# Optimization experiments

Hardware: AMD Instinct MI355X
Metric: run time of the kernel (lower is better)

Reference implementation:

```python
import jax, jax.numpy as jnp
import numpy as np

B, S, D, H = 4, 2048, 1024, 16
DEPTH = D // H
NEG = -1e10
BN_EPS = 1e-3


def setup_inputs() -> dict:
    key = jax.random.key(0)
    ks = jax.random.split(key, 6)
    scale = 0.02
    return {
        "x": jax.random.normal(ks[0], (B, S, D), dtype=jnp.float32),
        "mask": jax.random.randint(ks[1], (B, 1, 1, S), 0, 2, dtype=jnp.int32),
        "W_q": jax.random.normal(ks[2], (D, D), dtype=jnp.float32) * scale,
        "W_k": jax.random.normal(ks[3], (D, D), dtype=jnp.float32) * scale,
        "W_v": jax.random.normal(ks[4], (D, D), dtype=jnp.float32) * scale,
        "W_o": jax.random.normal(ks[5], (D, D), dtype=jnp.float32) * scale,
        "b_o": jnp.zeros((D,), dtype=jnp.float32),
        "gamma": jnp.ones((D,), dtype=jnp.float32),
        "beta": jnp.zeros((D,), dtype=jnp.float32),
        "moving_mean": jnp.zeros((D,), dtype=jnp.float32),
        "moving_var": jnp.ones((D,), dtype=jnp.float32),
    }


def _split_heads(t):
    # [B, S, D] -> [B, H, S, depth]
    return t.reshape(B, S, H, DEPTH).transpose(0, 2, 1, 3)


def reference(x, mask, W_q, W_k, W_v, W_o, b_o, gamma, beta, moving_mean, moving_var):
    Q = _split_heads(jnp.einsum("bsd,de->bse", x, W_q))
    K = _split_heads(jnp.einsum("bsd,de->bse", x, W_k))
    V = _split_heads(jnp.einsum("bsd,de->bse", x, W_v))
    # NOTE: scale is sqrt(EMBEDDING_SIZE), matching the original (not sqrt(depth)).
    scores = jnp.einsum("bhqd,bhkd->bhqk", Q, K) / jnp.sqrt(jnp.float32(D))
    # multiplicative mask: positions where mask==0 are multiplied by -1e10
    invalid = jnp.where(mask == 0, jnp.float32(NEG), jnp.float32(1.0))
    scores = scores * invalid
    attn = jax.nn.softmax(scores, axis=-1)
    out = jnp.einsum("bhqk,bhkd->bhqd", attn, V)
    out = out.transpose(0, 2, 1, 3).reshape(B, S, D)  # merge heads
    out = jnp.einsum("bsd,de->bse", out, W_o) + b_o
    # Keras BatchNormalization, inference mode (default call w/o training flag)
    out = gamma * (out - moving_mean) * jax.lax.rsqrt(moving_var + BN_EPS) + beta
    return out
```

## Files before the change

### kernel.cpp

```cpp
#include <hip/hip_runtime.h>
#include <hip/hip_bf16.h>
#include <float.h>

#define BB 4
#define SS 2048
#define DD 1024
#define HH 16
#define DP 64
#define BKS 32
#define MARGIN_F 0.025f
#define TIER2_TAU 1e-4

typedef __attribute__((ext_vector_type(8))) _Float16 half8v;
typedef __attribute__((ext_vector_type(16))) float f32x16;

typedef __attribute__((address_space(3))) void lds_void;
typedef const __attribute__((address_space(1))) void gbl_void;
static __device__ __forceinline__ void gload16(const void* g, void* l) {
  __builtin_amdgcn_global_load_lds((gbl_void*)g, (lds_void*)l, 16, 0, 0);
}

__global__ __launch_bounds__(256) void wtrans_kernel(
    const float* __restrict__ Wq, const float* __restrict__ Wk,
    const float* __restrict__ Wv, const float* __restrict__ Wo,
    _Float16* __restrict__ Wqh, _Float16* __restrict__ Wql,
    _Float16* __restrict__ Wkh, _Float16* __restrict__ Wkl,
    _Float16* __restrict__ Wvh, _Float16* __restrict__ Woh)
{
  const int z = blockIdx.z;
  const float* __restrict__ src = (z == 0) ? Wq : (z == 1 ? Wk : (z == 2 ? Wv : Wo));
  _Float16* __restrict__ dh = (z == 0) ? Wqh : (z == 1 ? Wkh : (z == 2 ? Wvh : Woh));
  _Float16* __restrict__ dl = (z == 0) ? Wql : Wkl;
  __shared__ float tile[64][65];
  const int k0 = blockIdx.x * 64, n0 = blockIdx.y * 64;
  const int c = threadIdx.x & 63, rb = threadIdx.x >> 6;
  #pragma unroll
  for (int i = 0; i < 16; ++i)
    tile[rb + 4 * i][c] = src[(size_t)(k0 + rb + 4 * i) * DD + n0 + c];
  __syncthreads();
  #pragma unroll
  for (int i = 0; i < 16; ++i) {
    const int n = n0 + rb + 4 * i;
    const float v = tile[c][rb + 4 * i];
    const _Float16 h = (_Float16)v;
    dh[(size_t)n * DD + k0 + c] = h;
    if (z < 2) dl[(size_t)n * DD + k0 + c] = (_Float16)(v - (float)h);
  }
}

__global__ __launch_bounds__(256) void proj_mfma(
    const float* __restrict__ x,
    const _Float16* __restrict__ Wqh, const _Float16* __restrict__ Wql,
    const _Float16* __restrict__ Wkh, const _Float16* __restrict__ Wkl,
    const _Float16* __restrict__ Wvh,
    _Float16* __restrict__ Qhi, _Float16* __restrict__ Qlo,
    _Float16* __restrict__ Khi, _Float16* __restrict__ Klo,
    _Float16* __restrict__ Vh)
{
  const int z = blockIdx.z;
  const bool split = (z < 2);
  const _Float16* __restrict__ Wh = (z == 0) ? Wqh : (z == 1 ? Wkh : Wvh);
  const _Float16* __restrict__ Wl = (z == 0) ? Wql : Wkl;
  _Float16* __restrict__ dhi = (z == 0) ? Qhi : (z == 1 ? Khi : Vh);
  _Float16* __restrict__ dlo = (z == 0) ? Qlo : Klo;

  __shared__ _Float16 Asm[8192];
  __shared__ _Float16 Bsm[8192];

  const int rows0 = blockIdx.x * 128, cols0 = blockIdx.y * 128;
  const int t = threadIdx.x;
  const int wid = t >> 6, l = t & 63;
  const int warpR = wid >> 1, warpC = wid & 1;
  const int lr = l & 31, lh = l >> 5;

  f32x16 acc[2][2];
  #pragma unroll
  for (int i = 0; i < 2; ++i)
    #pragma unroll
    for (int j = 0; j < 2; ++j)
      #pragma unroll
      for (int r = 0; r < 16; ++r) acc[i][j][r] = 0.f;

  const int arow = t >> 1;
  const int kc0 = (t & 1) * 2;
  const float* xsrc = x + (size_t)(rows0 + arow) * DD + kc0 * 8;
  int aslot_h0, aslot_h1, aslot_l0, aslot_l1;
  if (split) {
    aslot_h0 = arow * 8 + ((2 * kc0) ^ (arow & 7));
    aslot_h1 = arow * 8 + ((2 * kc0 + 2) ^ (arow & 7));
    aslot_l0 = arow * 8 + ((2 * kc0 + 1) ^ (arow & 7));
    aslot_l1 = arow * 8 + ((2 * kc0 + 3) ^ (arow & 7));
  } else {
    aslot_h0 = arow * 4 + (kc0 ^ ((arow >> 1) & 3));
    aslot_h1 = arow * 4 + ((kc0 + 1) ^ ((arow >> 1) & 3));
    aslot_l0 = aslot_l1 = 0;
  }

  const int nbi = split ? 4 : 2;
  const _Float16* bsrc[4];
  #pragma unroll
  for (int i = 0; i < 4; ++i) {
    const int s = t + i * 256;
    int col, wsrc; const _Float16* base;
    if (split) {
      col = s >> 3;
      const int u = (s & 7) ^ (col & 7);
      wsrc = u >> 1;
      base = (u & 1) ? Wl : Wh;
    } else {
      col = (s & 511) >> 2;
      wsrc = (s & 3) ^ ((col >> 1) & 3);
      base = Wh;
    }
    bsrc[i] = base + (size_t)(cols0 + col) * DD + wsrc * 8;
  }

  for (int ks = 0; ks < 32; ++ks) {
    const int k0 = ks * BKS;
    if (ks) __syncthreads();

    #pragma unroll
    for (int i = 0; i < 4; ++i)
      if (i < nbi) gload16(bsrc[i] + k0, &Bsm[(t + i * 256) * 8]);

    {
      const float4 f0 = *(const float4*)(xsrc + k0);
      const float4 f1 = *(const float4*)(xsrc + k0 + 4);
      const float4 f2 = *(const float4*)(xsrc + k0 + 8);
      const float4 f3 = *(const float4*)(xsrc + k0 + 12);
      const float xv[16] = {f0.x, f0.y, f0.z, f0.w, f1.x, f1.y, f1.z, f1.w,
                            f2.x, f2.y, f2.z, f2.w, f3.x, f3.y, f3.z, f3.w};
      half8v h0, h1, lo0, lo1;
      #pragma unroll
      for (int j = 0; j < 8; ++j) {
        h0[j] = (_Float16)xv[j];
        lo0[j] = (_Float16)(xv[j] - (float)h0[j]);
        h1[j] = (_Float16)xv[8 + j];
        lo1[j] = (_Float16)(xv[8 + j] - (float)h1[j]);
      }
      *(half8v*)&Asm[aslot_h0 * 8] = h0;
      *(half8v*)&Asm[aslot_h1 * 8] = h1;
      if (split) {
        *(half8v*)&Asm[aslot_l0 * 8] = lo0;
        *(half8v*)&Asm[aslot_l1 * 8] = lo1;
      }
    }
    __syncthreads();

    #pragma unroll
    for (int kh2 = 0; kh2 < 2; ++kh2) {
      const int c = kh2 * 2 + lh;
      half8v ah[2], alv[2], bh[2], blv[2];
      #pragma unroll
      for (int wr = 0; wr < 2; ++wr) {
        const int row = warpR * 64 + wr * 32 + lr;
        if (split) {
          ah[wr]  = *(const half8v*)&Asm[(row * 8 + ((2 * c) ^ (row & 7))) * 8];
          alv[wr] = *(const half8v*)&Asm[(row * 8 + ((2 * c + 1) ^ (row & 7))) * 8];
        } else {
          ah[wr] = *(const half8v*)&Asm[(row * 4 + (c ^ ((row >> 1) & 3))) * 8];
        }
      }
      #pragma unroll
      for (int wc = 0; wc < 2; ++wc) {
        const int col = warpC * 64 + wc * 32 + lr;
        if (split) {
          bh[wc]  = *(const half8v*)&Bsm[(col * 8 + ((2 * c) ^ (col & 7))) * 8];
          blv[wc] = *(const half8v*)&Bsm[(col * 8 + ((2 * c + 1) ^ (col & 7))) * 8];
        } else {
          bh[wc] = *(const half8v*)&Bsm[(col * 4 + (c ^ ((col >> 1) & 3))) * 8];
        }
      }
      #pragma unroll
      for (int wr = 0; wr < 2; ++wr)
        #pragma unroll
        for (int wc = 0; wc < 2; ++wc) {
          acc[wr][wc] = __builtin_amdgcn_mfma_f32_32x32x16_f16(ah[wr], bh[wc], acc[wr][wc], 0, 0, 0);
          if (split) {
            acc[wr][wc] = __builtin_amdgcn_mfma_f32_32x32x16_f16(alv[wr], bh[wc], acc[wr][wc], 0, 0, 0);
            acc[wr][wc] = __builtin_amdgcn_mfma_f32_32x32x16_f16(ah[wr], blv[wc], acc[wr][wc], 0, 0, 0);
          }
        }
    }
  }

  const int mb0 = rows0 + warpR * 64 + 4 * lh;
  #pragma unroll
  for (int wr = 0; wr < 2; ++wr)
    #pragma unroll
    for (int wc = 0; wc < 2; ++wc) {
      const int n = cols0 + warpC * 64 + wc * 32 + lr;
      const int h = n >> 6, d = n & 63;
      #pragma unroll
      for (int r = 0; r < 16; ++r) {
        const int m = mb0 + wr * 32 + (r & 3) + 8 * (r >> 2);
        const int b = m >> 11, srow = m & 2047;
        const size_t o = ((size_t)(b * HH + h) * SS + srow) * DP + d;
        const float a = acc[wr][wc][r];
        const _Float16 h16 = (_Float16)a;
        dhi[o] = h16;
        if (split) dlo[o] = (_Float16)(a - (float)h16);
      }
    }
}

__global__ __launch_bounds__(256) void scan_kernel(
    const int* __restrict__ mask, int* __restrict__ klist,
    int* __restrict__ cntpad, int* __restrict__ cntreal)
{
  __shared__ int part[256];
  __shared__ int tot;
  const int b = blockIdx.x, t = threadIdx.x;
  int loc[8]; int c = 0;
  #pragma unroll
  for (int j = 0; j < 8; ++j) {
    loc[j] = (mask[(b << 11) + t * 8 + j] == 0);
    c += loc[j];
  }
  part[t] = c;
  __syncthreads();
  if (t == 0) {
    int run = 0;
    for (int i = 0; i < 256; ++i) { int v = part[i]; part[i] = run; run += v; }
    tot = run;
  }
  __syncthreads();
  int off = part[t];
  #pragma unroll
  for (int j = 0; j < 8; ++j)
    if (loc[j]) klist[(b << 11) + off++] = t * 8 + j;
  __syncthreads();
  if (t == 0) {
    int n = tot;
    int first;
    if (n == 0) { klist[b << 11] = 0; n = 1; first = 0; }
    else first = klist[b << 11];
    int np = (n + 31) & ~31;
    for (int i = n; i < np; ++i) klist[(b << 11) + i] = first;
    cntpad[b] = np;
    cntreal[b] = n;
  }
}

__global__ __launch_bounds__(256) void filter_kernel(
    const _Float16* __restrict__ Qhi, const _Float16* __restrict__ Qlo,
    const _Float16* __restrict__ Khi,
    const int* __restrict__ klist, const int* __restrict__ cntpad,
    const int* __restrict__ cntreal,
    int* __restrict__ idx, int* __restrict__ ambr, int* __restrict__ ambc,
    int* __restrict__ cand, int* __restrict__ ccnt)
{
  __shared__ _Float16 Ksm[2048];
  const int bh = blockIdx.x >> 4;
  const int b = bh >> 4;
  const int wid = threadIdx.x >> 6;
  const int t = threadIdx.x;
  const int l = t & 63;
  const int q0 = ((blockIdx.x & 15) << 7) + (wid << 5);
  const int half = l >> 5;
  const int lq = l & 31;
  const int* __restrict__ kl_b = klist + (b << 11);

  half8v qh[4], ql[4];
  {
    const size_t qrow = ((size_t)bh * SS + q0 + lq) * DP + half * 8;
    #pragma unroll
    for (int ds = 0; ds < 4; ++ds) {
      qh[ds] = *(const half8v*)(Qhi + qrow + ds * 16);
      ql[ds] = *(const half8v*)(Qlo + qrow + ds * 16);
    }
  }

  const int srow = t >> 3;
  const int sslot = t & 7;
  const int scc = sslot ^ (srow & 7);

  const int nreal = cntreal[b];
  const int nt = cntpad[b] >> 5;
  float m1 = FLT_MAX, m2 = FLT_MAX, m3 = FLT_MAX, m4 = FLT_MAX;
  uint kidx[16];
  #pragma unroll
  for (int r = 0; r < 16; ++r)
    kidx[r] = (uint)((r & 3) + ((r >> 2) << 3) + (half << 2));

  const size_t kbase = (size_t)bh * SS;
  for (int kt = 0; kt < nt; ++kt) {
    if (kt) __syncthreads();
    {
      const int kval = kl_b[(kt << 5) + srow];
      gload16(Khi + (kbase + kval) * DP + scc * 8, &Ksm[t * 8]);
    }
    __syncthreads();

    f32x16 acc;
    #pragma unroll
    for (int r = 0; r < 16; ++r) acc[r] = 0.f;
    #pragma unroll
    for (int ds = 0; ds < 4; ++ds) {
      const int cc = ds * 2 + half;
      const int sl = lq * 8 + (cc ^ (lq & 7));
      const half8v kh = *(const half8v*)&Ksm[sl * 8];
      acc = __builtin_amdgcn_mfma_f32_32x32x16_f16(kh, qh[ds], acc, 0, 0, 0);
      acc = __builtin_amdgcn_mfma_f32_32x32x16_f16(kh, ql[ds], acc, 0, 0, 0);
    }
    const bool part = (kt == nt - 1) && ((nreal & 31) != 0);
    #pragma unroll
    for (int r = 0; r < 16; ++r) {
      const uint pv = (__float_as_uint(acc[r]) & 0xFFFFF800u) | kidx[r];
      float v = __uint_as_float(pv);
      if (part && kidx[r] >= (uint)nreal) v = FLT_MAX;
      m4 = __builtin_amdgcn_fmed3f(v, m3, m4);
      m3 = __builtin_amdgcn_fmed3f(v, m2, m3);
      m2 = __builtin_amdgcn_fmed3f(v, m1, m2);
      m1 = fminf(v, m1);
      kidx[r] += 32;
    }
  }

  float om[4];
  om[0] = __shfl_xor(m1, 32, 64);
  om[1] = __shfl_xor(m2, 32, 64);
  om[2] = __shfl_xor(m3, 32, 64);
  om[3] = __shfl_xor(m4, 32, 64);
  #pragma unroll
  for (int j = 0; j < 4; ++j) {
    const float v = om[j];
    m4 = __builtin_amdgcn_fmed3f(v, m3, m4);
    m3 = __builtin_amdgcn_fmed3f(v, m2, m3);
    m2 = __builtin_amdgcn_fmed3f(v, m1, m2);
    m1 = fminf(v, m1);
  }

  if (half == 0) {
    const int row = bh * SS + q0 + lq;
    const uint u1 = __float_as_uint(m1);
    const int k1 = kl_b[u1 & 2047u];
    idx[row] = k1;
    const float v1 = __uint_as_float(u1 & 0xFFFFF800u);
    const uint us[3] = {__float_as_uint(m2), __float_as_uint(m3),
                        __float_as_uint(m4)};
    const float v2 = __uint_as_float(us[0] & 0xFFFFF800u);
    if (v2 - v1 < MARGIN_F) {
      int c[4]; int n = 0;
      c[n++] = k1;
      #pragma unroll
      for (int j = 0; j < 3; ++j) {
        const float vj = __uint_as_float(us[j] & 0xFFFFF800u);
        if (vj - v1 < MARGIN_F) c[n++] = kl_b[us[j] & 2047u];
        else break;
      }
      const int pos = atomicAdd(ambc, 1);
      ambr[pos] = row;
      ccnt[row] = n;
      for (int j = 0; j < n; ++j) cand[row * 8 + j] = c[j];
    }
  }
}

__global__ __launch_bounds__(256) void refine_kernel(
    const _Float16* __restrict__ Qhi, const _Float16* __restrict__ Qlo,
    const _Float16* __restrict__ Khi, const _Float16* __restrict__ Klo,
    const float* __restrict__ x, const float* __restrict__ Wq,
    const float* __restrict__ Wk,
    const int* __restrict__ ambr, const int* __restrict__ ambc,
    const int* __restrict__ cand, const int* __restrict__ ccnt,
    int* __restrict__ idx)
{
  __shared__ double red[4][7][64];
  const int n = *ambc;
  const int t = threadIdx.x;
  const int w = t >> 6, lane = t & 63;

  for (int it = blockIdx.x; it < n; it += gridDim.x) {
    const int row = ambr[it];
    const int bh = row >> 11;
    const int cnum = ccnt[row];

    const size_t qb = (size_t)row * DP;
    const double q = (double)(float)Qhi[qb + lane] + (double)(float)Qlo[qb + lane];
    double best = 1e300, best2 = 1e300; int bi = 0x7fffffff;
    for (int c = 0; c < cnum; ++c) {
      const int k = cand[row * 8 + c] & 2047;
      const size_t kb = ((size_t)bh * SS + k) * DP;
      const double kv = (double)(float)Khi[kb + lane] + (double)(float)Klo[kb + lane];
      double p = q * kv;
      #pragma unroll
      for (int o = 32; o > 0; o >>= 1) p += __shfl_xor(p, o, 64);
      if (p < best) { best2 = best; best = p; bi = k; }
      else if (p < best2) best2 = p;
    }

    if (best2 - best < TIER2_TAU) {
      const int qq = row & 2047;
      const int b = bh >> 4, h = bh & 15;
      const int wc = (h << 6) + lane;
      const float* xq = x + ((size_t)(b << 11) + qq) * DD;
      int kk[6];
      #pragma unroll
      for (int c = 0; c < 6; ++c)
        kk[c] = cand[row * 8 + (c < cnum ? c : 0)] & 2047;
      const float* xk0 = x + ((size_t)(b << 11) + kk[0]) * DD;
      const float* xk1 = x + ((size_t)(b << 11) + kk[1]) * DD;
      const float* xk2 = x + ((size_t)(b << 11) + kk[2]) * DD;
      const float* xk3 = x + ((size_t)(b << 11) + kk[3]) * DD;
      const float* xk4 = x + ((size_t)(b << 11) + kk[4]) * DD;
      const float* xk5 = x + ((size_t)(b << 11) + kk[5]) * DD;

      double qd = 0.0, kd0 = 0.0, kd1 = 0.0, kd2 = 0.0,
             kd3 = 0.0, kd4 = 0.0, kd5 = 0.0;
      const int j0 = w * 256;
      #pragma unroll 4
      for (int j = j0; j < j0 + 256; ++j) {
        const double wq = (double)Wq[(size_t)j * DD + wc];
        const double wk = (double)Wk[(size_t)j * DD + wc];
        qd  = fma((double)xq[j],  wq, qd);
        kd0 = fma((double)xk0[j], wk, kd0);
        kd1 = fma((double)xk1[j], wk, kd1);
        kd2 = fma((double)xk2[j], wk, kd2);
        kd3 = fma((double)xk3[j], wk, kd3);
        kd4 = fma((double)xk4[j], wk, kd4);
        kd5 = fma((double)xk5[j], wk, kd5);
      }
      red[w][0][lane] = qd;
      red[w][1][lane] = kd0; red[w][2][lane] = kd1; red[w][3][lane] = kd2;
      red[w][4][lane] = kd3; red[w][5][lane] = kd4; red[w][6][lane] = kd5;
      __syncthreads();

      if (w == 0) {
        const double qs = red[0][0][lane] + red[1][0][lane] +
                          red[2][0][lane] + red[3][0][lane];
        best = 1e300; bi = 0x7fffffff;
        for (int c = 0; c < cnum; ++c) {
          const double ks = red[0][1 + c][lane] + red[1][1 + c][lane] +
                            red[2][1 + c][lane] + red[3][1 + c][lane];
          double p = qs * ks;
          #pragma unroll
          for (int o = 32; o > 0; o >>= 1) p += __shfl_xor(p, o, 64);
          const int k = kk[c];
          if (p < best || (p == best && k < bi)) { best = p; bi = k; }
        }
        if (lane == 0) idx[row] = bi;
      }
      __syncthreads();
    } else {
      if (t == 0) idx[row] = bi;
    }
  }
}

__global__ __launch_bounds__(256) void out_mfma(
    const _Float16* __restrict__ Vh, const int* __restrict__ idx,
    const _Float16* __restrict__ Woh, const float* __restrict__ bo,
    const float* __restrict__ gamma, const float* __restrict__ beta,
    const float* __restrict__ mmean, const float* __restrict__ mvar,
    float* __restrict__ out)
{
  __shared__ _Float16 Bsm[8192];
  const int rows0 = blockIdx.x * 128, cols0 = blockIdx.y * 128;
  const int t = threadIdx.x;
  const int w = t >> 6, l = t & 63;
  const int lr = l & 31, lh = l >> 5;
  const int hi8 = lh * 8;
  const int m = rows0 + w * 32 + lr;
  const int b = m >> 11, srow = m & 2047;

  const _Float16* bsrc[4];
  #pragma unroll
  for (int i = 0; i < 4; ++i) {
    const int s = t + i * 256;
    const int col = s >> 3;
    const int u = (s & 7) ^ (col & 7);
    bsrc[i] = Woh + (size_t)(cols0 + col) * DD + u * 8;
  }

  f32x16 acc[4];
  #pragma unroll
  for (int cf = 0; cf < 4; ++cf)
    #pragma unroll
    for (int r = 0; r < 16; ++r) acc[cf][r] = 0.f;

  for (int kt = 0; kt < 16; ++kt) {
    const int k0 = kt * 64;
    if (kt) __syncthreads();
    #pragma unroll
    for (int i = 0; i < 4; ++i)
      gload16(bsrc[i] + k0, &Bsm[(t + i * 256) * 8]);
    const int vi = idx[(size_t)(b * HH + kt) * SS + srow];
    const _Float16* arow = Vh + ((size_t)(b * HH + kt) * SS + vi) * DP;
    __syncthreads();

    #pragma unroll
    for (int ss = 0; ss < 4; ++ss) {
      half8v a = *(const half8v*)(arow + ss * 16 + hi8);
      const int cl = ss * 2 + lh;
      #pragma unroll
      for (int cf = 0; cf < 4; ++cf) {
        const int col = cf * 32 + lr;
        half8v bf = *(const half8v*)&Bsm[(col * 8 + (cl ^ (col & 7))) * 8];
        acc[cf] = __builtin_amdgcn_mfma_f32_32x32x16_f16(a, bf, acc[cf], 0, 0, 0);
      }
    }
  }

  const int m_base = rows0 + w * 32 + 4 * lh;
  #pragma unroll
  for (int cf = 0; cf < 4; ++cf) {
    const int n = cols0 + cf * 32 + lr;
    const float sc = gamma[n] * rsqrtf(mvar[n] + 1e-3f);
    const float ofs = (bo[n] - mmean[n]) * sc + beta[n];
    #pragma unroll
    for (int r = 0; r < 16; ++r) {
      const int mr = m_base + (r & 3) + 8 * (r >> 2);
      out[(size_t)mr * DD + n] = acc[cf][r] * sc + ofs;
    }
  }
}

extern "C" void kernel_launch(void* const* d_in, const int* in_sizes, int n_in,
                              void* d_out, int out_size, void* d_ws, size_t ws_size,
                              hipStream_t stream)
{
  const float* x  = (const float*)d_in[0];
  const int* mask = (const int*)d_in[1];
  const float* Wq = (const float*)d_in[2];
  const float* Wk = (const float*)d_in[3];
  const float* Wv = (const float*)d_in[4];
  const float* Wo = (const float*)d_in[5];
  const float* bo = (const float*)d_in[6];
  const float* ga = (const float*)d_in[7];
  const float* be = (const float*)d_in[8];
  const float* mm = (const float*)d_in[9];
  const float* mv = (const float*)d_in[10];
  float* out = (float*)d_out;

  char* ws = (char*)d_ws;
  _Float16* Qhi = (_Float16*)(ws + 0);
  _Float16* Qlo = (_Float16*)(ws + 16777216);
  _Float16* Khi = (_Float16*)(ws + 33554432);
  _Float16* Klo = (_Float16*)(ws + 50331648);
  _Float16* Vh  = (_Float16*)(ws + 67108864);
  _Float16* Wqh = (_Float16*)(ws + 83886080);
  _Float16* Wql = (_Float16*)(ws + 85983232);
  _Float16* Wkh = (_Float16*)(ws + 88080384);
  _Float16* Wkl = (_Float16*)(ws + 90177536);
  _Float16* Wvh = (_Float16*)(ws + 92274688);
  _Float16* Woh = (_Float16*)(ws + 94371840);
  int* klist    = (int*)(ws + 96468992);
  int* cntp     = (int*)(ws + 96501760);
  int* cntn     = (int*)(ws + 96501888);
  int* idx      = (int*)(ws + 96502016);
  int* ambr     = (int*)(ws + 97026304);
  int* ambc     = (int*)(ws + 97550592);
  int* ccnt     = (int*)(ws + 97550720);
  int* cnd      = (int*)(ws + 98075008);

  hipMemsetAsync(ambc, 0, 4, stream);
  wtrans_kernel<<<dim3(16, 16, 4), 256, 0, stream>>>(Wq, Wk, Wv, Wo,
                                                     Wqh, Wql, Wkh, Wkl, Wvh, Woh);
  scan_kernel<<<BB, 256, 0, stream>>>(mask, klist, cntp, cntn);
  proj_mfma<<<dim3(64, 8, 3), 256, 0, stream>>>(x, Wqh, Wql, Wkh, Wkl, Wvh,
                                                Qhi, Qlo, Khi, Klo, Vh);
  filter_kernel<<<1024, 256, 0, stream>>>(Qhi, Qlo, Khi, klist, cntp, cntn,
                                          idx, ambr, ambc, cnd, ccnt);
  refine_kernel<<<1024, 256, 0, stream>>>(Qhi, Qlo, Khi, Klo, x, Wq, Wk,
                                          ambr, ambc, cnd, ccnt, idx);
  out_mfma<<<dim3(64, 8), 256, 0, stream>>>(Vh, idx, Woh, bo, ga, be, mm, mv, out);
}
```

Baseline: 347.6 us.

## Precast x to fp16 hi/lo once and stream A tiles via direct LDS loads

```diff
diff --git a/kernel.cpp b/kernel.cpp
--- a/kernel.cpp
+++ b/kernel.cpp
@@ -20,14 +20,32 @@
   __builtin_amdgcn_global_load_lds((gbl_void*)g, (lds_void*)l, 16, 0, 0);
 }
 
+__global__ __launch_bounds__(256) void xcast_kernel(
+    const float* __restrict__ x, _Float16* __restrict__ xh,
+    _Float16* __restrict__ xl)
+{
+  const size_t e0 = ((size_t)blockIdx.x * 256 + threadIdx.x) * 8;
+  const float4 v0 = *(const float4*)(x + e0);
+  const float4 v1 = *(const float4*)(x + e0 + 4);
+  const float xv[8] = {v0.x, v0.y, v0.z, v0.w, v1.x, v1.y, v1.z, v1.w};
+  half8v h, l;
+  #pragma unroll
+  for (int j = 0; j < 8; ++j) {
+    h[j] = (_Float16)xv[j];
+    l[j] = (_Float16)(xv[j] - (float)h[j]);
+  }
+  *(half8v*)(xh + e0) = h;
+  *(half8v*)(xl + e0) = l;
+}
+
 __global__ __launch_bounds__(256) void wtrans_kernel(
     const float* __restrict__ Wq, const float* __restrict__ Wk,
     const float* __restrict__ Wv, const float* __restrict__ Wo,
     _Float16* __restrict__ Wqh, _Float16* __restrict__ Wql,
     _Float16* __restrict__ Wkh, _Float16* __restrict__ Wkl,
-    _Float16* __restrict__ Wvh, _Float16* __restrict__ Woh)
-{
-  const int z = blockIdx.z;
+    _Float16* __restrict__ Wvh, _Float16* __restrict__ Woh, int zofs)
+{
+  const int z = blockIdx.z + zofs;
   const float* __restrict__ src = (z == 0) ? Wq : (z == 1 ? Wk : (z == 2 ? Wv : Wo));
   _Float16* __restrict__ dh = (z == 0) ? Wqh : (z == 1 ? Wkh : (z == 2 ? Wvh : Woh));
   _Float16* __restrict__ dl = (z == 0) ? Wql : Wkl;
@@ -49,15 +67,15 @@
 }
 
 __global__ __launch_bounds__(256) void proj_mfma(
-    const float* __restrict__ x,
+    const _Float16* __restrict__ xh, const _Float16* __restrict__ xl,
     const _Float16* __restrict__ Wqh, const _Float16* __restrict__ Wql,
     const _Float16* __restrict__ Wkh, const _Float16* __restrict__ Wkl,
     const _Float16* __restrict__ Wvh,
     _Float16* __restrict__ Qhi, _Float16* __restrict__ Qlo,
     _Float16* __restrict__ Khi, _Float16* __restrict__ Klo,
-    _Float16* __restrict__ Vh)
-{
-  const int z = blockIdx.z;
+    _Float16* __restrict__ Vh, int zofs)
+{
+  const int z = blockIdx.z + zofs;
   const bool split = (z < 2);
   const _Float16* __restrict__ Wh = (z == 0) ? Wqh : (z == 1 ? Wkh : Wvh);
   const _Float16* __restrict__ Wl = (z == 0) ? Wql : Wkl;
@@ -81,38 +99,23 @@
       #pragma unroll
       for (int r = 0; r < 16; ++r) acc[i][j][r] = 0.f;
 
-  const int arow = t >> 1;
-  const int kc0 = (t & 1) * 2;
-  const float* xsrc = x + (size_t)(rows0 + arow) * DD + kc0 * 8;
-  int aslot_h0, aslot_h1, aslot_l0, aslot_l1;
-  if (split) {
-    aslot_h0 = arow * 8 + ((2 * kc0) ^ (arow & 7));
-    aslot_h1 = arow * 8 + ((2 * kc0 + 2) ^ (arow & 7));
-    aslot_l0 = arow * 8 + ((2 * kc0 + 1) ^ (arow & 7));
-    aslot_l1 = arow * 8 + ((2 * kc0 + 3) ^ (arow & 7));
-  } else {
-    aslot_h0 = arow * 4 + (kc0 ^ ((arow >> 1) & 3));
-    aslot_h1 = arow * 4 + ((kc0 + 1) ^ ((arow >> 1) & 3));
-    aslot_l0 = aslot_l1 = 0;
-  }
-
   const int nbi = split ? 4 : 2;
+  const _Float16* asrc[4];
   const _Float16* bsrc[4];
   #pragma unroll
   for (int i = 0; i < 4; ++i) {
     const int s = t + i * 256;
-    int col, wsrc; const _Float16* base;
     if (split) {
-      col = s >> 3;
-      const int u = (s & 7) ^ (col & 7);
-      wsrc = u >> 1;
-      base = (u & 1) ? Wl : Wh;
+      const int row = s >> 3;
+      const int u = (s & 7) ^ (row & 7);
+      asrc[i] = ((u & 1) ? xl : xh) + (size_t)(rows0 + row) * DD + (u >> 1) * 8;
+      bsrc[i] = ((u & 1) ? Wl : Wh) + (size_t)(cols0 + row) * DD + (u >> 1) * 8;
     } else {
-      col = (s & 511) >> 2;
-      wsrc = (s & 3) ^ ((col >> 1) & 3);
-      base = Wh;
-    }
-    bsrc[i] = base + (size_t)(cols0 + col) * DD + wsrc * 8;
+      const int row = (s & 511) >> 2;
+      const int csrc = (s & 3) ^ ((row >> 1) & 3);
+      asrc[i] = xh + (size_t)(rows0 + row) * DD + csrc * 8;
+      bsrc[i] = Wh + (size_t)(cols0 + row) * DD + csrc * 8;
+    }
   }
 
   for (int ks = 0; ks < 32; ++ks) {
@@ -121,30 +124,10 @@
 
     #pragma unroll
     for (int i = 0; i < 4; ++i)
-      if (i < nbi) gload16(bsrc[i] + k0, &Bsm[(t + i * 256) * 8]);
-
-    {
-      const float4 f0 = *(const float4*)(xsrc + k0);
-      const float4 f1 = *(const float4*)(xsrc + k0 + 4);
-      const float4 f2 = *(const float4*)(xsrc + k0 + 8);
-      const float4 f3 = *(const float4*)(xsrc + k0 + 12);
-      const float xv[16] = {f0.x, f0.y, f0.z, f0.w, f1.x, f1.y, f1.z, f1.w,
-                            f2.x, f2.y, f2.z, f2.w, f3.x, f3.y, f3.z, f3.w};
-      half8v h0, h1, lo0, lo1;
-      #pragma unroll
-      for (int j = 0; j < 8; ++j) {
-        h0[j] = (_Float16)xv[j];
-        lo0[j] = (_Float16)(xv[j] - (float)h0[j]);
-        h1[j] = (_Float16)xv[8 + j];
-        lo1[j] = (_Float16)(xv[8 + j] - (float)h1[j]);
-      }
-      *(half8v*)&Asm[aslot_h0 * 8] = h0;
-      *(half8v*)&Asm[aslot_h1 * 8] = h1;
-      if (split) {
-        *(half8v*)&Asm[aslot_l0 * 8] = lo0;
-        *(half8v*)&Asm[aslot_l1 * 8] = lo1;
-      }
-    }
+      if (i < nbi) {
+        gload16(asrc[i] + k0, &Asm[(t + i * 256) * 8]);
+        gload16(bsrc[i] + k0, &Bsm[(t + i * 256) * 8]);
+      }
     __syncthreads();
 
     #pragma unroll
@@ -534,32 +517,39 @@
   float* out = (float*)d_out;
 
   char* ws = (char*)d_ws;
-  _Float16* Qhi = (_Float16*)(ws + 0);
-  _Float16* Qlo = (_Float16*)(ws + 16777216);
-  _Float16* Khi = (_Float16*)(ws + 33554432);
-  _Float16* Klo = (_Float16*)(ws + 50331648);
-  _Float16* Vh  = (_Float16*)(ws + 67108864);
-  _Float16* Wqh = (_Float16*)(ws + 83886080);
-  _Float16* Wql = (_Float16*)(ws + 85983232);
-  _Float16* Wkh = (_Float16*)(ws + 88080384);
-  _Float16* Wkl = (_Float16*)(ws + 90177536);
-  _Float16* Wvh = (_Float16*)(ws + 92274688);
-  _Float16* Woh = (_Float16*)(ws + 94371840);
-  int* klist    = (int*)(ws + 96468992);
-  int* cntp     = (int*)(ws + 96501760);
-  int* cntn     = (int*)(ws + 96501888);
-  int* idx      = (int*)(ws + 96502016);
-  int* ambr     = (int*)(ws + 97026304);
-  int* ambc     = (int*)(ws + 97550592);
-  int* ccnt     = (int*)(ws + 97550720);
-  int* cnd      = (int*)(ws + 98075008);
-
+  _Float16* xh  = (_Float16*)(ws + 0);
+  _Float16* xl  = (_Float16*)(ws + 16777216);
+  _Float16* Vh  = (_Float16*)(ws + 16777216);
+  _Float16* Qhi = (_Float16*)(ws + 33554432);
+  _Float16* Qlo = (_Float16*)(ws + 50331648);
+  _Float16* Khi = (_Float16*)(ws + 67108864);
+  _Float16* Klo = (_Float16*)(ws + 83886080);
+  _Float16* Wqh = (_Float16*)(ws + 100663296);
+  _Float16* Wql = (_Float16*)(ws + 102760448);
+  _Float16* Wkh = (_Float16*)(ws + 104857600);
+  _Float16* Wkl = (_Float16*)(ws + 106954752);
+  _Float16* Wvh = (_Float16*)(ws + 109051904);
+  _Float16* Woh = (_Float16*)(ws + 0);
+  int* klist    = (int*)(ws + 2097152);
+  int* cntp     = (int*)(ws + 2129920);
+  int* cntn     = (int*)(ws + 2130048);
+  int* idx      = (int*)(ws + 2130176);
+  int* ambr     = (int*)(ws + 2654464);
+  int* ambc     = (int*)(ws + 3178752);
+  int* ccnt     = (int*)(ws + 3178880);
+  int* cnd      = (int*)(ws + 3703168);
+
+  wtrans_kernel<<<dim3(16, 16, 3), 256, 0, stream>>>(Wq, Wk, Wv, Wo,
+      Wqh, Wql, Wkh, Wkl, Wvh, Woh, 0);
+  xcast_kernel<<<4096, 256, 0, stream>>>(x, xh, xl);
+  proj_mfma<<<dim3(64, 8, 2), 256, 0, stream>>>(xh, xl, Wqh, Wql, Wkh, Wkl,
+      Wvh, Qhi, Qlo, Khi, Klo, Vh, 0);
+  proj_mfma<<<dim3(64, 8, 1), 256, 0, stream>>>(xh, xl, Wqh, Wql, Wkh, Wkl,
+      Wvh, Qhi, Qlo, Khi, Klo, Vh, 2);
+  wtrans_kernel<<<dim3(16, 16, 1), 256, 0, stream>>>(Wq, Wk, Wv, Wo,
+      Wqh, Wql, Wkh, Wkl, Wvh, Woh, 3);
+  scan_kernel<<<BB, 256, 0, stream>>>(mask, klist, cntp, cntn);
   hipMemsetAsync(ambc, 0, 4, stream);
-  wtrans_kernel<<<dim3(16, 16, 4), 256, 0, stream>>>(Wq, Wk, Wv, Wo,
-                                                     Wqh, Wql, Wkh, Wkl, Wvh, Woh);
-  scan_kernel<<<BB, 256, 0, stream>>>(mask, klist, cntp, cntn);
-  proj_mfma<<<dim3(64, 8, 3), 256, 0, stream>>>(x, Wqh, Wql, Wkh, Wkl, Wvh,
-                                                Qhi, Qlo, Khi, Klo, Vh);
   filter_kernel<<<1024, 256, 0, stream>>>(Qhi, Qlo, Khi, klist, cntp, cntn,
                                           idx, ambr, ambc, cnd, ccnt);
   refine_kernel<<<1024, 256, 0, stream>>>(Qhi, Qlo, Khi, Klo, x, Wq, Wk,
```

After: 368.0 us. +5.9%, slower.
